# Kernel optimization log

Measured on AMD Instinct MI355X. Metric: run time of the kernel, lower is better.

## Reference

```python
import jax, jax.numpy as jnp
import numpy as np

ORDER, IN_DIM, OUT_DIM, SEQ_LEN = 4096, 8, 1, 4096


def setup_inputs() -> dict:
    key = jax.random.key(0)
    ks = jax.random.split(key, 7)
    # reset_parameter uses uniform(-0.7, 0.7); A/C/L rescaled ~1/sqrt(order) for
    # numerical stability of the 4096-step linear recurrence (same math, stable values).
    sA = 0.9 * (3.0 / ORDER) ** 0.5
    sC = 0.7 / ORDER ** 0.5
    weight_a = jax.random.uniform(ks[0], (ORDER, ORDER), minval=-sA, maxval=sA, dtype=jnp.float32)
    weight_b = jax.random.uniform(ks[1], (ORDER, IN_DIM), minval=-0.7, maxval=0.7, dtype=jnp.float32)
    weight_c = jax.random.uniform(ks[2], (OUT_DIM, ORDER), minval=-sC, maxval=sC, dtype=jnp.float32)
    weight_d = jax.random.uniform(ks[3], (OUT_DIM, IN_DIM), minval=-0.7, maxval=0.7, dtype=jnp.float32)
    weight_l = jax.random.uniform(ks[4], (ORDER, 1), minval=-sC, maxval=sC, dtype=jnp.float32)
    u = jax.random.normal(ks[5], (IN_DIM, SEQ_LEN), dtype=jnp.float32)
    y_obs = jax.random.normal(ks[6], (1, SEQ_LEN), dtype=jnp.float32)
    return {"u": u, "y_obs": y_obs, "weight_a": weight_a, "weight_b": weight_b,
            "weight_c": weight_c, "weight_d": weight_d, "weight_l": weight_l}


def reference(u, y_obs, weight_a, weight_b, weight_c, weight_d, weight_l):
    # Observer (Luenberger) state-space recursion, inp_dim > 1 branch:
    #   y_t  = C h_t + D u_t
    #   h_{t+1} = A h_t + B u_t + L * (y_obs_t - y_t)
    # output = tanh(concat(y_t)) * 3, shape [out_dim, seq_len]
    order = weight_a.shape[0]
    h0 = jnp.ones((order, 1), dtype=u.dtype)  # nn.init.constant_(hidden, 1)

    def step(h, inp):
        u_t, yobs_t = inp  # u_t: [in_dim, 1], yobs_t: scalar
        y_t = weight_c @ h + weight_d @ u_t          # [out_dim, 1]
        h_next = weight_a @ h + weight_b @ u_t + weight_l * (yobs_t - y_t)
        return h_next, y_t

    u_seq = u.T[:, :, None]          # [seq_len, in_dim, 1]
    _, ys = jax.lax.scan(step, h0, (u_seq, y_obs[0]))
    y_hat = ys[:, :, 0].T            # [out_dim, seq_len]
    return jnp.tanh(y_hat) * 3
```

## Files before the change

kernel.cpp:

```cpp
#include <hip/hip_runtime.h>
#include <math.h>


constexpr int NDIM  = 4096;
constexpr int NC    = 10;
constexpr int SLAB  = 16 * 4096;
constexpr int JT    = 56;
constexpr int VAPPS = 28;
constexpr int KC    = NDIM / 32;
constexpr int TILES = NDIM / 16;

typedef float    f32x4  __attribute__((ext_vector_type(4)));
typedef _Float16 h16x8  __attribute__((ext_vector_type(8)));
typedef _Float16 f16;

__global__ __launch_bounds__(256) void k_build_a(
        const float* __restrict__ A, const float* __restrict__ C,
        const float* __restrict__ L, h16x8* __restrict__ AhSw) {
    const size_t idx = (size_t)blockIdx.x * blockDim.x + threadIdx.x;
    const int lane = (int)(idx & 63);
    const int kc   = (int)((idx >> 6) & (KC - 1));
    const int tile = (int)(idx >> 13);
    const int row  = tile * 16 + (lane & 15);
    const int col  = kc * 32 + (lane >> 4) * 8;
    const float4 a0 = *(const float4*)(A + (size_t)row * NDIM + col);
    const float4 a1 = *(const float4*)(A + (size_t)row * NDIM + col + 4);
    const float Li = L[row];
    union { h16x8 v; f16 h[8]; } pk;
    pk.h[0] = (f16)(a0.x - Li * C[col + 0]);
    pk.h[1] = (f16)(a0.y - Li * C[col + 1]);
    pk.h[2] = (f16)(a0.z - Li * C[col + 2]);
    pk.h[3] = (f16)(a0.w - Li * C[col + 3]);
    pk.h[4] = (f16)(a1.x - Li * C[col + 4]);
    pk.h[5] = (f16)(a1.y - Li * C[col + 5]);
    pk.h[6] = (f16)(a1.z - Li * C[col + 6]);
    pk.h[7] = (f16)(a1.w - Li * C[col + 7]);
    AhSw[idx] = pk.v;
}

__global__ __launch_bounds__(256) void k_build_w0(
        const float* __restrict__ Bm, const float* __restrict__ Dm,
        const float* __restrict__ L,
        float* __restrict__ Wf, f16* __restrict__ Wh) {
    int k = blockIdx.x * blockDim.x + threadIdx.x;
    float Lk = L[k];
    float col[16];
    #pragma unroll
    for (int c = 0; c < 8; ++c) col[c] = Bm[k * 8 + c] - Lk * Dm[c];
    col[8] = Lk; col[9] = 1.0f;
    #pragma unroll
    for (int c = 10; c < 16; ++c) col[c] = 0.0f;
    #pragma unroll
    for (int c = 0; c < 16; ++c) {
        Wf[c * NDIM + k] = col[c];
        Wh[c * NDIM + k] = (f16)col[c];
    }
}

__global__ __launch_bounds__(256) void k_stepVR(
        const h16x8* __restrict__ AhSw, const f16* __restrict__ WhIn,
        float* __restrict__ WfOut, f16* __restrict__ WhOut,
        const float* __restrict__ Cvec,
        const float* __restrict__ RpartIn, float* __restrict__ RpartOut,
        float* __restrict__ gfSlot, const int r) {
    const int tid = threadIdx.x;

    if (blockIdx.x < 256) {
        __shared__ f32x4 red[4][64];
        const int lane = tid & 63, wave = tid >> 6;
        const int mr   = lane & 15, q = lane >> 4;
        const int tile = blockIdx.x;
        const int row0 = tile * 16;
        const int k0   = wave * 1024;
        const bool liveB = (mr < NC);
        const h16x8* a8 = AhSw + ((size_t)tile * KC + wave * 32) * 64 + lane;
        const h16x8* b8 = (const h16x8*)WhIn + (((size_t)mr * NDIM + k0) >> 3) + q;

        f32x4 acc0 = {0,0,0,0}, acc1 = {0,0,0,0};
        for (int it = 0; it < 4; ++it) {
            h16x8 ra[8], rb[8];
            #pragma unroll
            for (int s = 0; s < 8; ++s) rb[s] = (h16x8){0,0,0,0,0,0,0,0};
            #pragma unroll
            for (int s = 0; s < 8; ++s) {
                const int c = it * 8 + s;
                ra[s] = a8[(size_t)c * 64];
            }
            if (liveB) {
                #pragma unroll
                for (int s = 0; s < 8; ++s) {
                    const int c = it * 8 + s;
                    rb[s] = b8[c * 4];
                }
            }
            #pragma unroll
            for (int s = 0; s < 8; ++s) {
                if (s & 1) acc1 = __builtin_amdgcn_mfma_f32_16x16x32_f16(ra[s], rb[s], acc1, 0, 0, 0);
                else       acc0 = __builtin_amdgcn_mfma_f32_16x16x32_f16(ra[s], rb[s], acc0, 0, 0, 0);
            }
        }
        red[wave][lane] = acc0 + acc1;
        __syncthreads();
        if (tid < 64) {
            f32x4 v = red[0][tid] + red[1][tid] + red[2][tid] + red[3][tid];
            const int col = tid & 15;
            if (col < NC) {
                const int rb0 = row0 + ((tid >> 4) << 2);
                #pragma unroll
                for (int i = 0; i < 4; ++i) {
                    WfOut[col * NDIM + rb0 + i] = v[i];
                    WhOut[col * NDIM + rb0 + i] = (f16)v[i];
                }
            }
        }
    } else {
        __shared__ float rp[256][17];
        __shared__ float g2[16][17];
        __shared__ float gs[16];
        const int t = blockIdx.x - 256;

        if (r == 0) {
            if (tid < 16) gs[tid] = Cvec[t * 16 + tid];
        } else {
            const float* src = RpartIn + (size_t)tid * NDIM + t * 16;
            #pragma unroll
            for (int j = 0; j < 16; j += 4) {
                float4 v = *(const float4*)(src + j);
                rp[tid][j] = v.x; rp[tid][j+1] = v.y;
                rp[tid][j+2] = v.z; rp[tid][j+3] = v.w;
            }
            __syncthreads();
            {
                const int c = tid & 15, g = tid >> 4;
                float p = 0.0f;
                #pragma unroll
                for (int j = 0; j < 16; ++j) p += rp[g * 16 + j][c];
                g2[g][c] = p;
            }
            __syncthreads();
            if (tid < 16) {
                float s = 0.0f;
                #pragma unroll
                for (int g = 0; g < 16; ++g) s += g2[g][tid];
                gs[tid] = s;
            }
        }
        __syncthreads();
        if (tid < 16) gfSlot[t * 16 + tid] = gs[tid];

        if (r < VAPPS - 1) {
            float gloc[16];
            #pragma unroll
            for (int j = 0; j < 16; ++j) gloc[j] = gs[j];
            const h16x8* base = AhSw + (size_t)t * (KC * 64);
            #pragma unroll
            for (int cc = 0; cc < 2; ++cc) {
                const int ch = tid * 2 + cc;
                const h16x8* fr = base + (size_t)ch * 16;
                float acc[8] = {};
                #pragma unroll
                for (int mrr = 0; mrr < 16; ++mrr) {
                    union { h16x8 v; f16 h[8]; } ua;
                    ua.v = fr[mrr];
                    const float gm = gloc[mrr];
                    #pragma unroll
                    for (int j = 0; j < 8; ++j) acc[j] += gm * (float)ua.h[j];
                }
                float4* op = (float4*)(RpartOut + (size_t)t * NDIM + 8 * ch);
                op[0] = make_float4(acc[0], acc[1], acc[2], acc[3]);
                op[1] = make_float4(acc[4], acc[5], acc[6], acc[7]);
            }
        }
    }
}

__global__ __launch_bounds__(256) void k_fbatch(
        const float* __restrict__ Wall, const float* __restrict__ C,
        const float* __restrict__ gf, float* __restrict__ F) {
    const int m = blockIdx.x;
    const float* W;
    const float* vec;
    if (m <= VAPPS) { W = Wall + (size_t)m * SLAB;     vec = C; }
    else            { W = Wall + (size_t)VAPPS * SLAB; vec = gf + (size_t)(m - VAPPS) * NDIM; }
    const int tid = threadIdx.x, lane = tid & 63, wave = tid >> 6;
    float acc[NC] = {};
    for (int k = tid; k < NDIM; k += 256) {
        float ck = vec[k];
        #pragma unroll
        for (int c = 0; c < NC; ++c) acc[c] += ck * W[c * NDIM + k];
    }
    __shared__ float red[4][NC];
    #pragma unroll
    for (int c = 0; c < NC; ++c) {
        float s = acc[c];
        #pragma unroll
        for (int off = 32; off > 0; off >>= 1) s += __shfl_down(s, off);
        if (lane == 0) red[wave][c] = s;
    }
    __syncthreads();
    if (tid < NC) F[m * NC + tid] = red[0][tid] + red[1][tid] + red[2][tid] + red[3][tid];
}

__global__ __launch_bounds__(256) void k_conv(
        const float* __restrict__ F, const float* __restrict__ u,
        const float* __restrict__ yobs, const float* __restrict__ Dm,
        float* __restrict__ out) {
    __shared__ float Fl[JT * NC];
    __shared__ float zw[(JT + 256) * 9];
    const int tid = threadIdx.x;
    const int t0  = blockIdx.x * 256;
    for (int idx = tid; idx < JT * NC; idx += 256) Fl[idx] = F[idx];
    for (int idx = tid; idx < (JT + 256) * 9; idx += 256) {
        int k = idx / 9, c = idx - k * 9;
        int s = t0 - JT + k;
        float v = 0.0f;
        if (s >= 0 && s < NDIM) v = (c < 8) ? u[c * NDIM + s] : yobs[s];
        zw[idx] = v;
    }
    __syncthreads();
    const int t = t0 + tid;
    float y = (t < JT) ? Fl[t * NC + 9] : 0.0f;
    #pragma unroll
    for (int c = 0; c < 8; ++c) y += Dm[c] * u[c * NDIM + t];
    for (int j = 0; j < JT; ++j) {
        const float* fj = Fl + j * NC;
        const float* zz = zw + (tid + JT - 1 - j) * 9;
        float p = 0.0f;
        #pragma unroll
        for (int c = 0; c < 9; ++c) p += fj[c] * zz[c];
        y += p;
    }
    out[t] = 3.0f * tanhf(y);
}

extern "C" void kernel_launch(void* const* d_in, const int* in_sizes, int n_in,
                              void* d_out, int out_size, void* d_ws, size_t ws_size,
                              hipStream_t stream) {
    const float* u    = (const float*)d_in[0];
    const float* yobs = (const float*)d_in[1];
    const float* A    = (const float*)d_in[2];
    const float* Bm   = (const float*)d_in[3];
    const float* C    = (const float*)d_in[4];
    const float* Dm   = (const float*)d_in[5];
    const float* L    = (const float*)d_in[6];
    float* out = (float*)d_out;

    char* ws = (char*)d_ws;
    h16x8* AhSw  = (h16x8*)ws;
    float* Wf    = (float*)(ws + 33554432ull);
    f16*   Wh    = (f16*)(ws + 41156608ull);
    float* gf    = (float*)(ws + 44957696ull);
    float* Rpart = (float*)(ws + 45416448ull);
    float* F     = (float*)(ws + 53805056ull);

    constexpr size_t RPN = (size_t)256 * NDIM;

    k_build_a<<<dim3(TILES * KC * 64 / 256), dim3(256), 0, stream>>>(A, C, L, AhSw);
    k_build_w0<<<dim3(16), dim3(256), 0, stream>>>(Bm, Dm, L, Wf, Wh);

    for (int r = 0; r < VAPPS; ++r) {
        const size_t in   = (size_t)r * SLAB;
        const size_t out_ = (size_t)(r + 1) * SLAB;
        const float* rin  = Rpart + ((r + 1) & 1) * RPN;
        float*       rout = Rpart + (r & 1) * RPN;
        k_stepVR<<<dim3(512), dim3(256), 0, stream>>>(
            AhSw, Wh + in, Wf + out_, Wh + out_,
            C, rin, rout, gf + (size_t)r * NDIM, r);
    }

    k_fbatch<<<dim3(JT), dim3(256), 0, stream>>>(Wf, C, gf, F);
    k_conv<<<dim3(16), dim3(256), 0, stream>>>(F, u, yobs, Dm, out);
}
```

Before: 470.8 us.

## Halve step-kernel grid, give each block two tiles, and tile A-build via LDS

k_build_a now stages 64x64 tiles of A - L*C in shared memory so global reads are coalesced row-wise before writing the swizzled fp16 layout. k_stepVR drops from 512 to 256 blocks: each MFMA block handles two row tiles with a two-way K split, and each reduction/vector block handles 32 rows and reads two tiles of A. The Rpart partial buffer shrinks from 256 to 128 slices, which also moves the F workspace offset. Fewer blocks per launch may lower per-step overhead and reduction traffic, but it also cuts parallelism across the CUs.

```diff
diff --git a/kernel.cpp b/kernel.cpp
--- a/kernel.cpp
+++ b/kernel.cpp
@@ -17,25 +17,31 @@
 __global__ __launch_bounds__(256) void k_build_a(
         const float* __restrict__ A, const float* __restrict__ C,
         const float* __restrict__ L, h16x8* __restrict__ AhSw) {
-    const size_t idx = (size_t)blockIdx.x * blockDim.x + threadIdx.x;
-    const int lane = (int)(idx & 63);
-    const int kc   = (int)((idx >> 6) & (KC - 1));
-    const int tile = (int)(idx >> 13);
-    const int row  = tile * 16 + (lane & 15);
-    const int col  = kc * 32 + (lane >> 4) * 8;
-    const float4 a0 = *(const float4*)(A + (size_t)row * NDIM + col);
-    const float4 a1 = *(const float4*)(A + (size_t)row * NDIM + col + 4);
-    const float Li = L[row];
-    union { h16x8 v; f16 h[8]; } pk;
-    pk.h[0] = (f16)(a0.x - Li * C[col + 0]);
-    pk.h[1] = (f16)(a0.y - Li * C[col + 1]);
-    pk.h[2] = (f16)(a0.z - Li * C[col + 2]);
-    pk.h[3] = (f16)(a0.w - Li * C[col + 3]);
-    pk.h[4] = (f16)(a1.x - Li * C[col + 4]);
-    pk.h[5] = (f16)(a1.y - Li * C[col + 5]);
-    pk.h[6] = (f16)(a1.z - Li * C[col + 6]);
-    pk.h[7] = (f16)(a1.w - Li * C[col + 7]);
-    AhSw[idx] = pk.v;
+    __shared__ float lds[64][65];
+    const int R0 = (blockIdx.x & 63) * 64;
+    const int C0 = (blockIdx.x >> 6) * 64;
+    const int tid = threadIdx.x;
+    #pragma unroll
+    for (int it = 0; it < 16; ++it) {
+        const int r = it * 4 + (tid >> 6);
+        const int c = tid & 63;
+        lds[r][c] = A[(size_t)(R0 + r) * NDIM + C0 + c]
+                  - L[R0 + r] * C[C0 + c];
+    }
+    __syncthreads();
+    #pragma unroll
+    for (int half = 0; half < 2; ++half) {
+        const int o = half * 256 + tid;
+        const int r = o >> 3;
+        const int g = o & 7;
+        union { h16x8 v; f16 h[8]; } pk;
+        #pragma unroll
+        for (int j = 0; j < 8; ++j) pk.h[j] = (f16)lds[r][g * 8 + j];
+        const int tile = (R0 >> 4) + (r >> 4);
+        const int kc   = (C0 >> 5) + (g >> 2);
+        const int lane = (r & 15) | ((g & 3) << 4);
+        AhSw[((size_t)tile * KC + kc) * 64 + lane] = pk.v;
+    }
 }
 
 __global__ __launch_bounds__(256) void k_build_w0(
@@ -65,19 +71,20 @@
         float* __restrict__ gfSlot, const int r) {
     const int tid = threadIdx.x;
 
-    if (blockIdx.x < 256) {
+    if (blockIdx.x < 128) {
         __shared__ f32x4 red[4][64];
         const int lane = tid & 63, wave = tid >> 6;
         const int mr   = lane & 15, q = lane >> 4;
-        const int tile = blockIdx.x;
-        const int row0 = tile * 16;
-        const int k0   = wave * 1024;
+        const int tp   = blockIdx.x;
+        const int tile = tp * 2 + (wave >> 1);
+        const int kh   = wave & 1;
+        const int k0   = kh * 2048;
         const bool liveB = (mr < NC);
-        const h16x8* a8 = AhSw + ((size_t)tile * KC + wave * 32) * 64 + lane;
+        const h16x8* a8 = AhSw + ((size_t)tile * KC + kh * 64) * 64 + lane;
         const h16x8* b8 = (const h16x8*)WhIn + (((size_t)mr * NDIM + k0) >> 3) + q;
 
         f32x4 acc0 = {0,0,0,0}, acc1 = {0,0,0,0};
-        for (int it = 0; it < 4; ++it) {
+        for (int it = 0; it < 8; ++it) {
             h16x8 ra[8], rb[8];
             #pragma unroll
             for (int s = 0; s < 8; ++s) rb[s] = (h16x8){0,0,0,0,0,0,0,0};
@@ -101,11 +108,14 @@
         }
         red[wave][lane] = acc0 + acc1;
         __syncthreads();
-        if (tid < 64) {
-            f32x4 v = red[0][tid] + red[1][tid] + red[2][tid] + red[3][tid];
-            const int col = tid & 15;
+        if (tid < 128) {
+            const int half = tid >> 6;
+            const int l    = tid & 63;
+            f32x4 v = red[half * 2][l] + red[half * 2 + 1][l];
+            const int col = l & 15;
             if (col < NC) {
-                const int rb0 = row0 + ((tid >> 4) << 2);
+                const int row0 = (tp * 2 + half) * 16;
+                const int rb0  = row0 + ((l >> 4) << 2);
                 #pragma unroll
                 for (int i = 0; i < 4; ++i) {
                     WfOut[col * NDIM + rb0 + i] = v[i];
@@ -114,57 +124,58 @@
             }
         }
     } else {
-        __shared__ float rp[256][17];
-        __shared__ float g2[16][17];
-        __shared__ float gs[16];
-        const int t = blockIdx.x - 256;
+        __shared__ float rp[4096];
+        __shared__ float g8[8][33];
+        __shared__ float gs[32];
+        const int t = blockIdx.x - 128;
 
         if (r == 0) {
-            if (tid < 16) gs[tid] = Cvec[t * 16 + tid];
+            if (tid < 32) gs[tid] = Cvec[t * 32 + tid];
         } else {
-            const float* src = RpartIn + (size_t)tid * NDIM + t * 16;
-            #pragma unroll
-            for (int j = 0; j < 16; j += 4) {
-                float4 v = *(const float4*)(src + j);
-                rp[tid][j] = v.x; rp[tid][j+1] = v.y;
-                rp[tid][j+2] = v.z; rp[tid][j+3] = v.w;
+            #pragma unroll
+            for (int i = 0; i < 16; ++i) {
+                const int idx = tid + i * 256;
+                rp[idx] = RpartIn[(size_t)(idx >> 5) * NDIM + t * 32 + (idx & 31)];
             }
             __syncthreads();
             {
-                const int c = tid & 15, g = tid >> 4;
-                float p = 0.0f;
-                #pragma unroll
-                for (int j = 0; j < 16; ++j) p += rp[g * 16 + j][c];
-                g2[g][c] = p;
+                const int c = tid & 31, g = tid >> 5;
+                float s = 0.0f;
+                #pragma unroll
+                for (int j = 0; j < 16; ++j) s += rp[(g * 16 + j) * 32 + c];
+                g8[g][c] = s;
             }
             __syncthreads();
-            if (tid < 16) {
+            if (tid < 32) {
                 float s = 0.0f;
                 #pragma unroll
-                for (int g = 0; g < 16; ++g) s += g2[g][tid];
+                for (int g = 0; g < 8; ++g) s += g8[g][tid];
                 gs[tid] = s;
             }
         }
         __syncthreads();
-        if (tid < 16) gfSlot[t * 16 + tid] = gs[tid];
+        if (tid < 32) gfSlot[t * 32 + tid] = gs[tid];
 
         if (r < VAPPS - 1) {
-            float gloc[16];
-            #pragma unroll
-            for (int j = 0; j < 16; ++j) gloc[j] = gs[j];
-            const h16x8* base = AhSw + (size_t)t * (KC * 64);
+            float gl[32];
+            #pragma unroll
+            for (int j = 0; j < 32; ++j) gl[j] = gs[j];
             #pragma unroll
             for (int cc = 0; cc < 2; ++cc) {
                 const int ch = tid * 2 + cc;
-                const h16x8* fr = base + (size_t)ch * 16;
                 float acc[8] = {};
                 #pragma unroll
-                for (int mrr = 0; mrr < 16; ++mrr) {
-                    union { h16x8 v; f16 h[8]; } ua;
-                    ua.v = fr[mrr];
-                    const float gm = gloc[mrr];
+                for (int tt = 0; tt < 2; ++tt) {
+                    const h16x8* fr = AhSw + (size_t)(t * 2 + tt) * (KC * 64)
+                                    + (size_t)ch * 16;
                     #pragma unroll
-                    for (int j = 0; j < 8; ++j) acc[j] += gm * (float)ua.h[j];
+                    for (int mrr = 0; mrr < 16; ++mrr) {
+                        union { h16x8 v; f16 h[8]; } ua;
+                        ua.v = fr[mrr];
+                        const float gm = gl[tt * 16 + mrr];
+                        #pragma unroll
+                        for (int j = 0; j < 8; ++j) acc[j] += gm * (float)ua.h[j];
+                    }
                 }
                 float4* op = (float4*)(RpartOut + (size_t)t * NDIM + 8 * ch);
                 op[0] = make_float4(acc[0], acc[1], acc[2], acc[3]);
@@ -251,11 +262,11 @@
     f16*   Wh    = (f16*)(ws + 41156608ull);
     float* gf    = (float*)(ws + 44957696ull);
     float* Rpart = (float*)(ws + 45416448ull);
-    float* F     = (float*)(ws + 53805056ull);
-
-    constexpr size_t RPN = (size_t)256 * NDIM;
-
-    k_build_a<<<dim3(TILES * KC * 64 / 256), dim3(256), 0, stream>>>(A, C, L, AhSw);
+    float* F     = (float*)(ws + 49610752ull);
+
+    constexpr size_t RPN = (size_t)128 * NDIM;
+
+    k_build_a<<<dim3(64 * 64), dim3(256), 0, stream>>>(A, C, L, AhSw);
     k_build_w0<<<dim3(16), dim3(256), 0, stream>>>(Bm, Dm, L, Wf, Wh);
 
     for (int r = 0; r < VAPPS; ++r) {
@@ -263,7 +274,7 @@
         const size_t out_ = (size_t)(r + 1) * SLAB;
         const float* rin  = Rpart + ((r + 1) & 1) * RPN;
         float*       rout = Rpart + (r & 1) * RPN;
-        k_stepVR<<<dim3(512), dim3(256), 0, stream>>>(
+        k_stepVR<<<dim3(256), dim3(256), 0, stream>>>(
             AhSw, Wh + in, Wf + out_, Wh + out_,
             C, rin, rout, gf + (size_t)r * NDIM, r);
     }
```

Result: no change. 462.3 us (-1.8%).
